# Kernel optimization log

Measured on AMD Instinct MI355X. Metric: run time of the kernel, lower is better.

The kernel has to match this reference:

```python
import jax, jax.numpy as jnp
import numpy as np

LAMBDA = 0.5
TAU = 1.0
EPS = 1e-8  # torch F.cosine_similarity eps

B, D = 8192, 1024


def setup_inputs() -> dict:
    key = jax.random.key(0)
    k1, k2, k3, k4 = jax.random.split(key, 4)
    return {
        "student_query_emb": jax.random.normal(k1, (B, D), dtype=jnp.float32),
        "student_passage_emb": jax.random.normal(k2, (B, D), dtype=jnp.float32),
        "teacher_query_emb": jax.random.normal(k3, (B, D), dtype=jnp.float32),
        "teacher_passage_emb": jax.random.normal(k4, (B, D), dtype=jnp.float32),
    }


def _mse(a, b):
    d = a - b
    return jnp.mean(d * d)


def _retrieval_loss(q, p):
    # cosine sim = (q . p) / max(||q|| * ||p||, eps); normalize then matmul
    # (avoids the [B,B,D] broadcast intermediate of the torch version)
    qn = q / jnp.maximum(jnp.linalg.norm(q, axis=-1, keepdims=True), EPS)
    pn = p / jnp.maximum(jnp.linalg.norm(p, axis=-1, keepdims=True), EPS)
    logits = jnp.einsum("bd,cd->bc", qn, pn) / TAU  # [B, B]
    # cross-entropy with labels = arange(B): pick the diagonal log-prob
    logprobs = jax.nn.log_softmax(logits, axis=-1)
    return -jnp.mean(jnp.diagonal(logprobs))


def reference(student_query_emb, student_passage_emb, teacher_query_emb, teacher_passage_emb):
    distill = 0.5 * (_mse(student_query_emb, teacher_query_emb)
                     + _mse(student_passage_emb, teacher_passage_emb))
    retrieval = _retrieval_loss(student_query_emb, student_passage_emb)
    return LAMBDA * distill + (1.0 - LAMBDA) * retrieval
```

## Files before the change

### kernel.cpp

```cpp
#include <hip/hip_runtime.h>
#include <hip/hip_bf16.h>

typedef unsigned short u16;
typedef unsigned char u8;
typedef float f32x4 __attribute__((ext_vector_type(4)));
typedef int int4v __attribute__((ext_vector_type(4)));
typedef int int8v __attribute__((ext_vector_type(8)));

#define B_ROWS 8192
#define D_DIM  1024
#define FP8_SCALE 16.0f
#define ACC_UNSCALE (1.0f/256.0f)


__global__ void __launch_bounds__(256) prep_kernel(
    const float* __restrict__ sq, const float* __restrict__ sp,
    const float* __restrict__ tq, const float* __restrict__ tp,
    int* __restrict__ qn, int* __restrict__ pn,
    float* __restrict__ ppq, float* __restrict__ ppp, float* __restrict__ ppd)
{
    const int r = blockIdx.x;
    const int t = threadIdx.x;
    const size_t base4 = (size_t)r * (D_DIM / 4) + t;

    const float4 q = ((const float4*)sq)[base4];
    const float4 p = ((const float4*)sp)[base4];
    const float4 a = ((const float4*)tq)[base4];
    const float4 b = ((const float4*)tp)[base4];

    float sq2 = q.x*q.x + q.y*q.y + q.z*q.z + q.w*q.w;
    float sp2 = p.x*p.x + p.y*p.y + p.z*p.z + p.w*p.w;
    float dqx = q.x-a.x, dqy = q.y-a.y, dqz = q.z-a.z, dqw = q.w-a.w;
    float dq  = dqx*dqx + dqy*dqy + dqz*dqz + dqw*dqw;
    float dpx = p.x-b.x, dpy = p.y-b.y, dpz = p.z-b.z, dpw = p.w-b.w;
    float dp  = dpx*dpx + dpy*dpy + dpz*dpz + dpw*dpw;
    float qp  = q.x*p.x + q.y*p.y + q.z*p.z + q.w*p.w;

    #pragma unroll
    for (int m = 1; m <= 32; m <<= 1) {
        sq2 += __shfl_xor(sq2, m);
        sp2 += __shfl_xor(sp2, m);
        dq  += __shfl_xor(dq, m);
        dp  += __shfl_xor(dp, m);
        qp  += __shfl_xor(qp, m);
    }

    __shared__ float red[4][5];
    const int wave = t >> 6, lane = t & 63;
    if (lane == 0) {
        red[wave][0] = sq2; red[wave][1] = sp2;
        red[wave][2] = dq;  red[wave][3] = dp; red[wave][4] = qp;
    }
    __syncthreads();

    const float S0 = red[0][0] + red[1][0] + red[2][0] + red[3][0];
    const float S1 = red[0][1] + red[1][1] + red[2][1] + red[3][1];
    const float rq = 1.0f / fmaxf(sqrtf(S0), 1e-8f);
    const float rp = 1.0f / fmaxf(sqrtf(S1), 1e-8f);

    if (t == 0) {
        float S2 = red[0][2] + red[1][2] + red[2][2] + red[3][2];
        float S3 = red[0][3] + red[1][3] + red[2][3] + red[3][3];
        float S4 = red[0][4] + red[1][4] + red[2][4] + red[3][4];
        ppq[r] = S2;
        ppp[r] = S3;
        ppd[r] = S4 * rq * rp;
    }

    const float fq = rq * FP8_SCALE;
    const float fp = rp * FP8_SCALE;
    int pkq = __builtin_amdgcn_cvt_pk_fp8_f32(q.x * fq, q.y * fq, 0, false);
    pkq     = __builtin_amdgcn_cvt_pk_fp8_f32(q.z * fq, q.w * fq, pkq, true);
    int pkp = __builtin_amdgcn_cvt_pk_fp8_f32(p.x * fp, p.y * fp, 0, false);
    pkp     = __builtin_amdgcn_cvt_pk_fp8_f32(p.z * fp, p.w * fp, pkp, true);
    qn[base4] = pkq;
    pn[base4] = pkp;
}

__global__ void __launch_bounds__(256) gemm_rowsum_kernel(
    const u8* __restrict__ Q, const u8* __restrict__ P,
    float* __restrict__ gpart)
{
    __shared__ u8 smA[128 * 128];
    __shared__ u8 smB[128 * 128];

    const int tid  = threadIdx.x;
    const int wave = tid >> 6;
    const int lane = tid & 63;
    const int bm = blockIdx.y;
    const int bn = blockIdx.x;

    const int lrow   = lane >> 3;
    const int gchunk = (lane & 7) ^ lrow;
    const u8* Ag = Q + ((size_t)bm * 128) * D_DIM + gchunk * 16;
    const u8* Bg = P + ((size_t)bn * 128) * D_DIM + gchunk * 16;

    const int quad  = lane >> 4;
    const int rw    = lane & 15;
    const int r7    = lane & 7;
    const int arow0 = (wave >> 1) * 64;
    const int bcol0 = (wave & 1) * 64;

    const int off_lo = ((2 * quad) ^ r7) * 16;
    const int off_hi = ((2 * quad + 1) ^ r7) * 16;

    f32x4 acc[4][4];
    #pragma unroll
    for (int i = 0; i < 4; ++i)
        #pragma unroll
        for (int j = 0; j < 4; ++j)
            acc[i][j] = (f32x4){0.f, 0.f, 0.f, 0.f};

    for (int k0 = 0; k0 < D_DIM; k0 += 128) {
        #pragma unroll
        for (int i = 0; i < 4; ++i) {
            const int r0 = wave * 32 + i * 8;
            __builtin_amdgcn_global_load_lds(
                (const __attribute__((address_space(1))) void*)(Ag + (size_t)(r0 + lrow) * D_DIM + k0),
                (__attribute__((address_space(3))) void*)(smA + r0 * 128), 16, 0, 0);
            __builtin_amdgcn_global_load_lds(
                (const __attribute__((address_space(1))) void*)(Bg + (size_t)(r0 + lrow) * D_DIM + k0),
                (__attribute__((address_space(3))) void*)(smB + r0 * 128), 16, 0, 0);
        }
        __syncthreads();

        int8v afrag[4], bfrag[4];
        #pragma unroll
        for (int mi = 0; mi < 4; ++mi) {
            const u8* row = smA + (arow0 + mi * 16 + rw) * 128;
            int4v lo = *(const int4v*)(row + off_lo);
            int4v hi = *(const int4v*)(row + off_hi);
            afrag[mi] = __builtin_shufflevector(lo, hi, 0, 1, 2, 3, 4, 5, 6, 7);
        }
        #pragma unroll
        for (int ni = 0; ni < 4; ++ni) {
            const u8* row = smB + (bcol0 + ni * 16 + rw) * 128;
            int4v lo = *(const int4v*)(row + off_lo);
            int4v hi = *(const int4v*)(row + off_hi);
            bfrag[ni] = __builtin_shufflevector(lo, hi, 0, 1, 2, 3, 4, 5, 6, 7);
        }
        #pragma unroll
        for (int mi = 0; mi < 4; ++mi)
            #pragma unroll
            for (int ni = 0; ni < 4; ++ni)
                acc[mi][ni] = __builtin_amdgcn_mfma_scale_f32_16x16x128_f8f6f4(
                    afrag[mi], bfrag[ni], acc[mi][ni],
                    0, 0,
                    0, 0x7f7f7f7f,
                    0, 0x7f7f7f7f);
        __syncthreads();
    }

    float esum[4][4];
    #pragma unroll
    for (int mi = 0; mi < 4; ++mi)
        #pragma unroll
        for (int r = 0; r < 4; ++r) {
            float s = 0.f;
            #pragma unroll
            for (int ni = 0; ni < 4; ++ni)
                s += __expf(acc[mi][ni][r] * ACC_UNSCALE);
            esum[mi][r] = s;
        }
    #pragma unroll
    for (int m = 1; m <= 8; m <<= 1)
        #pragma unroll
        for (int mi = 0; mi < 4; ++mi)
            #pragma unroll
            for (int r = 0; r < 4; ++r)
                esum[mi][r] += __shfl_xor(esum[mi][r], m);

    if (rw == 0) {
        float* dst = gpart + ((size_t)(bn * 2 + (wave & 1))) * B_ROWS
                   + bm * 128 + arow0;
        #pragma unroll
        for (int mi = 0; mi < 4; ++mi)
            #pragma unroll
            for (int r = 0; r < 4; ++r)
                dst[mi * 16 + quad * 4 + r] = esum[mi][r];
    }
}

__global__ void __launch_bounds__(256) reduce_kernel(
    const float* __restrict__ gpart, float* __restrict__ lsp)
{
    const int r = blockIdx.x * 256 + threadIdx.x;
    float s = 0.f;
    #pragma unroll 8
    for (int j = 0; j < 128; ++j) s += gpart[(size_t)j * B_ROWS + r];
    float ls = logf(s);
    #pragma unroll
    for (int m = 1; m <= 32; m <<= 1) ls += __shfl_xor(ls, m);
    __shared__ float red[4];
    const int t = threadIdx.x;
    if ((t & 63) == 0) red[t >> 6] = ls;
    __syncthreads();
    if (t == 0) lsp[blockIdx.x] = red[0] + red[1] + red[2] + red[3];
}

__global__ void __launch_bounds__(256) finalize_kernel(
    const float* __restrict__ ppq, const float* __restrict__ ppp,
    const float* __restrict__ ppd, const float* __restrict__ lsp,
    float* __restrict__ out)
{
    const int t = threadIdx.x;
    float s2 = 0.f, s3 = 0.f, s4 = 0.f;
    for (int i = t; i < B_ROWS; i += 256) {
        s2 += ppq[i]; s3 += ppp[i]; s4 += ppd[i];
    }
    float lt = (t < 32) ? lsp[t] : 0.f;
    #pragma unroll
    for (int m = 1; m <= 32; m <<= 1) {
        s2 += __shfl_xor(s2, m);
        s3 += __shfl_xor(s3, m);
        s4 += __shfl_xor(s4, m);
        lt += __shfl_xor(lt, m);
    }
    __shared__ float red[4][4];
    if ((t & 63) == 0) {
        red[t >> 6][0] = s2; red[t >> 6][1] = s3;
        red[t >> 6][2] = s4; red[t >> 6][3] = lt;
    }
    __syncthreads();
    if (t == 0) {
        float S2 = red[0][0] + red[1][0] + red[2][0] + red[3][0];
        float S3 = red[0][1] + red[1][1] + red[2][1] + red[3][1];
        float S4 = red[0][2] + red[1][2] + red[2][2] + red[3][2];
        float LT = red[0][3] + red[1][3] + red[2][3] + red[3][3];
        const float inv_bd = 1.0f / ((float)B_ROWS * (float)D_DIM);
        float distill   = 0.5f * (S2 + S3) * inv_bd;
        float retrieval = (LT - S4) / (float)B_ROWS;
        out[0] = 0.5f * distill + 0.5f * retrieval;
    }
}

extern "C" void kernel_launch(void* const* d_in, const int* in_sizes, int n_in,
                              void* d_out, int out_size, void* d_ws, size_t ws_size,
                              hipStream_t stream) {
    const float* sq = (const float*)d_in[0];
    const float* sp = (const float*)d_in[1];
    const float* tq = (const float*)d_in[2];
    const float* tp = (const float*)d_in[3];

    char* ws = (char*)d_ws;
    float* ppq   = (float*)(ws);
    float* ppp   = (float*)(ws + 32768);
    float* ppd   = (float*)(ws + 65536);
    float* lsp   = (float*)(ws + 98304);
    float* gpart = (float*)(ws + 131072);
    int*   qn    = (int*)(ws + 131072 + (size_t)128 * B_ROWS * 4);
    int*   pn    = (int*)((char*)qn + (size_t)B_ROWS * D_DIM);

    prep_kernel<<<B_ROWS, 256, 0, stream>>>(sq, sp, tq, tp, qn, pn, ppq, ppp, ppd);
    gemm_rowsum_kernel<<<dim3(64, 64), 256, 0, stream>>>((const u8*)qn, (const u8*)pn, gpart);
    reduce_kernel<<<32, 256, 0, stream>>>(gpart, lsp);
    finalize_kernel<<<1, 256, 0, stream>>>(ppq, ppp, ppd, lsp, (float*)d_out);
}
```

Baseline: 253.5 us.

## Use one wave per row in prep, split LDS fragment loads, fold per-row sums into reduce

The prep kernel now gives each wave one row, so a block handles four rows and the shared-memory reduction and block barrier go away. Each lane loads four float4 chunks of each input and keeps the q/p values in registers for the FP8 packing. In the GEMM, the low halves of all A/B fragments are read from LDS before the high halves, with a sched_barrier between them, to change how LDS reads are issued. The per-row distill and dot sums move from the single-block finalize into the 32-block reduce kernel, leaving a tiny 64-thread finalize.

New measurement: 244.1 us. 1.04x faster.

```diff
diff --git a/kernel.cpp b/kernel.cpp
--- a/kernel.cpp
+++ b/kernel.cpp
@@ -19,22 +19,31 @@
     int* __restrict__ qn, int* __restrict__ pn,
     float* __restrict__ ppq, float* __restrict__ ppp, float* __restrict__ ppd)
 {
-    const int r = blockIdx.x;
-    const int t = threadIdx.x;
-    const size_t base4 = (size_t)r * (D_DIM / 4) + t;
-
-    const float4 q = ((const float4*)sq)[base4];
-    const float4 p = ((const float4*)sp)[base4];
-    const float4 a = ((const float4*)tq)[base4];
-    const float4 b = ((const float4*)tp)[base4];
-
-    float sq2 = q.x*q.x + q.y*q.y + q.z*q.z + q.w*q.w;
-    float sp2 = p.x*p.x + p.y*p.y + p.z*p.z + p.w*p.w;
-    float dqx = q.x-a.x, dqy = q.y-a.y, dqz = q.z-a.z, dqw = q.w-a.w;
-    float dq  = dqx*dqx + dqy*dqy + dqz*dqz + dqw*dqw;
-    float dpx = p.x-b.x, dpy = p.y-b.y, dpz = p.z-b.z, dpw = p.w-b.w;
-    float dp  = dpx*dpx + dpy*dpy + dpz*dpz + dpw*dpw;
-    float qp  = q.x*p.x + q.y*p.y + q.z*p.z + q.w*p.w;
+    const int wave = threadIdx.x >> 6;
+    const int l    = threadIdx.x & 63;
+    const int r    = blockIdx.x * 4 + wave;
+    const size_t rb4 = (size_t)r * (D_DIM / 4);
+
+    const float4* Q4 = (const float4*)sq + rb4;
+    const float4* P4 = (const float4*)sp + rb4;
+    const float4* A4 = (const float4*)tq + rb4;
+    const float4* B4 = (const float4*)tp + rb4;
+
+    float4 qv[4], pv[4];
+    float sq2 = 0.f, sp2 = 0.f, dq = 0.f, dp = 0.f, qp = 0.f;
+    #pragma unroll
+    for (int j = 0; j < 4; ++j) {
+        const int idx = j * 64 + l;
+        float4 q = Q4[idx], p = P4[idx], a = A4[idx], b = B4[idx];
+        qv[j] = q; pv[j] = p;
+        sq2 += q.x*q.x + q.y*q.y + q.z*q.z + q.w*q.w;
+        sp2 += p.x*p.x + p.y*p.y + p.z*p.z + p.w*p.w;
+        float dx = q.x-a.x, dy = q.y-a.y, dz = q.z-a.z, dw = q.w-a.w;
+        dq += dx*dx + dy*dy + dz*dz + dw*dw;
+        dx = p.x-b.x; dy = p.y-b.y; dz = p.z-b.z; dw = p.w-b.w;
+        dp += dx*dx + dy*dy + dz*dz + dw*dw;
+        qp += q.x*p.x + q.y*p.y + q.z*p.z + q.w*p.w;
+    }
 
     #pragma unroll
     for (int m = 1; m <= 32; m <<= 1) {
@@ -45,36 +54,29 @@
         qp  += __shfl_xor(qp, m);
     }
 
-    __shared__ float red[4][5];
-    const int wave = t >> 6, lane = t & 63;
-    if (lane == 0) {
-        red[wave][0] = sq2; red[wave][1] = sp2;
-        red[wave][2] = dq;  red[wave][3] = dp; red[wave][4] = qp;
-    }
-    __syncthreads();
-
-    const float S0 = red[0][0] + red[1][0] + red[2][0] + red[3][0];
-    const float S1 = red[0][1] + red[1][1] + red[2][1] + red[3][1];
-    const float rq = 1.0f / fmaxf(sqrtf(S0), 1e-8f);
-    const float rp = 1.0f / fmaxf(sqrtf(S1), 1e-8f);
-
-    if (t == 0) {
-        float S2 = red[0][2] + red[1][2] + red[2][2] + red[3][2];
-        float S3 = red[0][3] + red[1][3] + red[2][3] + red[3][3];
-        float S4 = red[0][4] + red[1][4] + red[2][4] + red[3][4];
-        ppq[r] = S2;
-        ppp[r] = S3;
-        ppd[r] = S4 * rq * rp;
+    const float rq = 1.0f / fmaxf(sqrtf(sq2), 1e-8f);
+    const float rp = 1.0f / fmaxf(sqrtf(sp2), 1e-8f);
+
+    if (l == 0) {
+        ppq[r] = dq;
+        ppp[r] = dp;
+        ppd[r] = qp * rq * rp;
     }
 
     const float fq = rq * FP8_SCALE;
     const float fp = rp * FP8_SCALE;
-    int pkq = __builtin_amdgcn_cvt_pk_fp8_f32(q.x * fq, q.y * fq, 0, false);
-    pkq     = __builtin_amdgcn_cvt_pk_fp8_f32(q.z * fq, q.w * fq, pkq, true);
-    int pkp = __builtin_amdgcn_cvt_pk_fp8_f32(p.x * fp, p.y * fp, 0, false);
-    pkp     = __builtin_amdgcn_cvt_pk_fp8_f32(p.z * fp, p.w * fp, pkp, true);
-    qn[base4] = pkq;
-    pn[base4] = pkp;
+    int* qrow = qn + (size_t)r * (D_DIM / 4);
+    int* prow = pn + (size_t)r * (D_DIM / 4);
+    #pragma unroll
+    for (int j = 0; j < 4; ++j) {
+        const int idx = j * 64 + l;
+        int pk = __builtin_amdgcn_cvt_pk_fp8_f32(qv[j].x * fq, qv[j].y * fq, 0, false);
+        pk     = __builtin_amdgcn_cvt_pk_fp8_f32(qv[j].z * fq, qv[j].w * fq, pk, true);
+        qrow[idx] = pk;
+        pk = __builtin_amdgcn_cvt_pk_fp8_f32(pv[j].x * fp, pv[j].y * fp, 0, false);
+        pk = __builtin_amdgcn_cvt_pk_fp8_f32(pv[j].z * fp, pv[j].w * fp, pk, true);
+        prow[idx] = pk;
+    }
 }
 
 __global__ void __launch_bounds__(256) gemm_rowsum_kernel(
@@ -124,27 +126,28 @@
         }
         __syncthreads();
 
-        int8v afrag[4], bfrag[4];
-        #pragma unroll
-        for (int mi = 0; mi < 4; ++mi) {
-            const u8* row = smA + (arow0 + mi * 16 + rw) * 128;
-            int4v lo = *(const int4v*)(row + off_lo);
-            int4v hi = *(const int4v*)(row + off_hi);
-            afrag[mi] = __builtin_shufflevector(lo, hi, 0, 1, 2, 3, 4, 5, 6, 7);
-        }
-        #pragma unroll
-        for (int ni = 0; ni < 4; ++ni) {
-            const u8* row = smB + (bcol0 + ni * 16 + rw) * 128;
-            int4v lo = *(const int4v*)(row + off_lo);
-            int4v hi = *(const int4v*)(row + off_hi);
-            bfrag[ni] = __builtin_shufflevector(lo, hi, 0, 1, 2, 3, 4, 5, 6, 7);
-        }
+        union Frag { int8v v8; struct { int4v lo, hi; } h; };
+        Frag af[4], bf[4];
+        #pragma unroll
+        for (int mi = 0; mi < 4; ++mi)
+            af[mi].h.lo = *(const int4v*)(smA + (arow0 + mi * 16 + rw) * 128 + off_lo);
+        #pragma unroll
+        for (int ni = 0; ni < 4; ++ni)
+            bf[ni].h.lo = *(const int4v*)(smB + (bcol0 + ni * 16 + rw) * 128 + off_lo);
+        __builtin_amdgcn_sched_barrier(0);
+        #pragma unroll
+        for (int mi = 0; mi < 4; ++mi)
+            af[mi].h.hi = *(const int4v*)(smA + (arow0 + mi * 16 + rw) * 128 + off_hi);
+        #pragma unroll
+        for (int ni = 0; ni < 4; ++ni)
+            bf[ni].h.hi = *(const int4v*)(smB + (bcol0 + ni * 16 + rw) * 128 + off_hi);
+
         #pragma unroll
         for (int mi = 0; mi < 4; ++mi)
             #pragma unroll
             for (int ni = 0; ni < 4; ++ni)
                 acc[mi][ni] = __builtin_amdgcn_mfma_scale_f32_16x16x128_f8f6f4(
-                    afrag[mi], bfrag[ni], acc[mi][ni],
+                    af[mi].v8, bf[ni].v8, acc[mi][ni],
                     0, 0,
                     0, 0x7f7f7f7f,
                     0, 0x7f7f7f7f);
@@ -182,54 +185,56 @@
 }
 
 __global__ void __launch_bounds__(256) reduce_kernel(
-    const float* __restrict__ gpart, float* __restrict__ lsp)
-{
-    const int r = blockIdx.x * 256 + threadIdx.x;
+    const float* __restrict__ gpart,
+    const float* __restrict__ ppq, const float* __restrict__ ppp,
+    const float* __restrict__ ppd, float4* __restrict__ bpart)
+{
+    const int t = threadIdx.x;
+    const int r = blockIdx.x * 256 + t;
     float s = 0.f;
     #pragma unroll 8
     for (int j = 0; j < 128; ++j) s += gpart[(size_t)j * B_ROWS + r];
     float ls = logf(s);
-    #pragma unroll
-    for (int m = 1; m <= 32; m <<= 1) ls += __shfl_xor(ls, m);
-    __shared__ float red[4];
-    const int t = threadIdx.x;
-    if ((t & 63) == 0) red[t >> 6] = ls;
-    __syncthreads();
-    if (t == 0) lsp[blockIdx.x] = red[0] + red[1] + red[2] + red[3];
-}
-
-__global__ void __launch_bounds__(256) finalize_kernel(
-    const float* __restrict__ ppq, const float* __restrict__ ppp,
-    const float* __restrict__ ppd, const float* __restrict__ lsp,
-    float* __restrict__ out)
-{
-    const int t = threadIdx.x;
-    float s2 = 0.f, s3 = 0.f, s4 = 0.f;
-    for (int i = t; i < B_ROWS; i += 256) {
-        s2 += ppq[i]; s3 += ppp[i]; s4 += ppd[i];
-    }
-    float lt = (t < 32) ? lsp[t] : 0.f;
+    float v2 = ppq[r], v3 = ppp[r], v4 = ppd[r];
     #pragma unroll
     for (int m = 1; m <= 32; m <<= 1) {
-        s2 += __shfl_xor(s2, m);
-        s3 += __shfl_xor(s3, m);
-        s4 += __shfl_xor(s4, m);
-        lt += __shfl_xor(lt, m);
+        ls += __shfl_xor(ls, m);
+        v2 += __shfl_xor(v2, m);
+        v3 += __shfl_xor(v3, m);
+        v4 += __shfl_xor(v4, m);
     }
     __shared__ float red[4][4];
     if ((t & 63) == 0) {
-        red[t >> 6][0] = s2; red[t >> 6][1] = s3;
-        red[t >> 6][2] = s4; red[t >> 6][3] = lt;
+        red[t >> 6][0] = ls; red[t >> 6][1] = v2;
+        red[t >> 6][2] = v3; red[t >> 6][3] = v4;
     }
     __syncthreads();
     if (t == 0) {
-        float S2 = red[0][0] + red[1][0] + red[2][0] + red[3][0];
-        float S3 = red[0][1] + red[1][1] + red[2][1] + red[3][1];
-        float S4 = red[0][2] + red[1][2] + red[2][2] + red[3][2];
-        float LT = red[0][3] + red[1][3] + red[2][3] + red[3][3];
+        float4 o;
+        o.x = red[0][0] + red[1][0] + red[2][0] + red[3][0];
+        o.y = red[0][1] + red[1][1] + red[2][1] + red[3][1];
+        o.z = red[0][2] + red[1][2] + red[2][2] + red[3][2];
+        o.w = red[0][3] + red[1][3] + red[2][3] + red[3][3];
+        bpart[blockIdx.x] = o;
+    }
+}
+
+__global__ void __launch_bounds__(64) finalize_kernel(
+    const float4* __restrict__ bpart, float* __restrict__ out)
+{
+    const int t = threadIdx.x;
+    float4 v = (t < 32) ? bpart[t] : (float4){0.f, 0.f, 0.f, 0.f};
+    #pragma unroll
+    for (int m = 1; m <= 16; m <<= 1) {
+        v.x += __shfl_xor(v.x, m);
+        v.y += __shfl_xor(v.y, m);
+        v.z += __shfl_xor(v.z, m);
+        v.w += __shfl_xor(v.w, m);
+    }
+    if (t == 0) {
         const float inv_bd = 1.0f / ((float)B_ROWS * (float)D_DIM);
-        float distill   = 0.5f * (S2 + S3) * inv_bd;
-        float retrieval = (LT - S4) / (float)B_ROWS;
+        float distill   = 0.5f * (v.y + v.z) * inv_bd;
+        float retrieval = (v.x - v.w) / (float)B_ROWS;
         out[0] = 0.5f * distill + 0.5f * retrieval;
     }
 }
@@ -243,16 +248,16 @@
     const float* tp = (const float*)d_in[3];
 
     char* ws = (char*)d_ws;
-    float* ppq   = (float*)(ws);
-    float* ppp   = (float*)(ws + 32768);
-    float* ppd   = (float*)(ws + 65536);
-    float* lsp   = (float*)(ws + 98304);
-    float* gpart = (float*)(ws + 131072);
-    int*   qn    = (int*)(ws + 131072 + (size_t)128 * B_ROWS * 4);
-    int*   pn    = (int*)((char*)qn + (size_t)B_ROWS * D_DIM);
-
-    prep_kernel<<<B_ROWS, 256, 0, stream>>>(sq, sp, tq, tp, qn, pn, ppq, ppp, ppd);
+    float*  ppq   = (float*)(ws);
+    float*  ppp   = (float*)(ws + 32768);
+    float*  ppd   = (float*)(ws + 65536);
+    float4* bpart = (float4*)(ws + 98304);
+    float*  gpart = (float*)(ws + 131072);
+    int*    qn    = (int*)(ws + 131072 + (size_t)128 * B_ROWS * 4);
+    int*    pn    = (int*)((char*)qn + (size_t)B_ROWS * D_DIM);
+
+    prep_kernel<<<B_ROWS / 4, 256, 0, stream>>>(sq, sp, tq, tp, qn, pn, ppq, ppp, ppd);
     gemm_rowsum_kernel<<<dim3(64, 64), 256, 0, stream>>>((const u8*)qn, (const u8*)pn, gpart);
-    reduce_kernel<<<32, 256, 0, stream>>>(gpart, lsp);
-    finalize_kernel<<<1, 256, 0, stream>>>(ppq, ppp, ppd, lsp, (float*)d_out);
-}
+    reduce_kernel<<<32, 256, 0, stream>>>(gpart, ppq, ppp, ppd, bpart);
+    finalize_kernel<<<1, 64, 0, stream>>>(bpart, (float*)d_out);
+}
```
